# Kernel optimization log

Measured on AMD Instinct MI355X. Metric: run time of the kernel, lower is better.

Reference implementation:

```python
import jax, jax.numpy as jnp
import numpy as np

B, T, C = 4, 1024, 1024
N_HEAD = 16
MEMORY = 64  # sliding-window size: key j visible to query i iff 0 <= i-j <= MEMORY


def setup_inputs() -> dict:
    key = jax.random.key(0)
    k1, k2, k3 = jax.random.split(key, 3)
    x = jax.random.normal(k1, (B, T, C), dtype=jnp.float32)
    # torch Linear weight is [out, in]; we store transposed [in, out] for x @ W
    W_attn = jax.random.normal(k2, (C, 3 * C), dtype=jnp.float32) * (1.0 / np.sqrt(C))
    W_proj = jax.random.normal(k3, (C, C), dtype=jnp.float32) * (1.0 / np.sqrt(C))
    return {"x": x, "W_attn": W_attn, "W_proj": W_proj}


def reference(x, W_attn, W_proj):
    Bv, Tv, Cv = x.shape
    hd = Cv // N_HEAD
    qkv = x @ W_attn                               # [B,T,3C]
    q, k, v = jnp.split(qkv, 3, axis=-1)
    def heads(t):
        return t.reshape(Bv, Tv, N_HEAD, hd).transpose(0, 2, 1, 3)  # [B,H,T,hd]
    q, k, v = heads(q), heads(k), heads(v)
    scale = 1.0 / np.sqrt(hd)
    scores = jnp.einsum('bhqd,bhkd->bhqk', q, k) * scale            # [B,H,T,T]
    i = jnp.arange(Tv)
    diff = i[:, None] - i[None, :]                                  # i - j
    band_mask = (diff >= 0) & (diff <= MEMORY)                      # M1 * ~M2
    y = jax.nn.softmax(jnp.where(band_mask, scores, -jnp.inf), axis=-1) @ v
    # get_att=True path: full causal attention probabilities (no window)
    att = jax.nn.softmax(jnp.where(diff >= 0, scores, -jnp.inf), axis=-1)
    att_std = jnp.std(att, axis=0, ddof=1)                          # torch .std default ddof=1
    y = y.transpose(0, 2, 1, 3).reshape(Bv, Tv, Cv)
    y = y @ W_proj
    return (y, att, att_std)
```

## Files before the change

kernel.cpp:

```cpp
#include <hip/hip_runtime.h>
#include <hip/hip_bf16.h>
#include <stdint.h>

#define Bb 4
#define Tt 1024
#define Hh 16
#define HD 64
#define C3 3072
#define WIN 64

typedef __bf16 bf16x8 __attribute__((ext_vector_type(8)));
typedef float f32x4 __attribute__((ext_vector_type(4)));

#define MFMA16(a, b, c) __builtin_amdgcn_mfma_f32_16x16x32_bf16((a), (b), (c), 0, 0, 0)

static __device__ __forceinline__ unsigned short f2bf(float f) {
  union { float f; unsigned u; } v; v.f = f;
  unsigned r = (v.u + 0x7FFFu + ((v.u >> 16) & 1u)) >> 16;
  return (unsigned short)r;
}
static __device__ __forceinline__ float bf2f(unsigned short h) {
  union { unsigned u; float f; } v; v.u = ((unsigned)h) << 16;
  return v.f;
}

__global__ __launch_bounds__(256) void k_convert(const float* __restrict__ in,
                                                 unsigned short* __restrict__ out, int n4) {
  int i = blockIdx.x * 256 + threadIdx.x;
  if (i >= n4) return;
  float4 v = ((const float4*)in)[i];
  ushort4 o;
  o.x = f2bf(v.x); o.y = f2bf(v.y); o.z = f2bf(v.z); o.w = f2bf(v.w);
  ((ushort4*)out)[i] = o;
}

__global__ __launch_bounds__(256) void k_transconv(const float* __restrict__ Win,
                                                   unsigned short* __restrict__ Wt,
                                                   int K, int N) {
  __shared__ float tile[32][33];
  int n0 = blockIdx.x * 32, k0 = blockIdx.y * 32;
  int tx = threadIdx.x & 31, ty = threadIdx.x >> 5;
  for (int r = ty; r < 32; r += 8)
    tile[r][tx] = Win[(size_t)(k0 + r) * N + n0 + tx];
  __syncthreads();
  for (int r = ty; r < 32; r += 8)
    Wt[(size_t)(n0 + r) * K + k0 + tx] = f2bf(tile[tx][r]);
}

template <int BF16_OUT, int SCALEQ>
__global__ __launch_bounds__(256) void k_gemm_bt(const unsigned short* __restrict__ A,
                                                 const unsigned short* __restrict__ Bt,
                                                 void* __restrict__ Cv, int M, int N, int K) {
  __shared__ unsigned short lds[2 * 128 * 32];
  unsigned short* as_ = lds;
  unsigned short* bs_ = lds + 128 * 32;
  const int tid = threadIdx.x;
  const int m0 = blockIdx.x * 128, n0 = blockIdx.y * 128;
  const int w = tid >> 6, lane = tid & 63;
  const int wm = (w >> 1) * 64, wn = (w & 1) * 64;
  const int lrow = lane & 15, lk = lane >> 4;

  f32x4 z = {0.f, 0.f, 0.f, 0.f};
  f32x4 acc[4][4];
#pragma unroll
  for (int i = 0; i < 4; ++i)
#pragma unroll
    for (int j = 0; j < 4; ++j) acc[i][j] = z;

  const int nk = K >> 5;
  for (int kt = 0; kt < nk; ++kt) {
    const int k0 = kt << 5;
    __syncthreads();
#pragma unroll
    for (int p = 0; p < 2; ++p) {
      int seg = tid + p * 256;
      int row = seg >> 2, ks = (seg & 3) << 3;
      __builtin_amdgcn_global_load_lds(
          (__attribute__((address_space(1))) void*)(A + (size_t)(m0 + row) * K + k0 + ks),
          (__attribute__((address_space(3))) void*)(as_ + seg * 8), 16, 0, 0);
      __builtin_amdgcn_global_load_lds(
          (__attribute__((address_space(1))) void*)(Bt + (size_t)(n0 + row) * K + k0 + ks),
          (__attribute__((address_space(3))) void*)(bs_ + seg * 8), 16, 0, 0);
    }
    __syncthreads();
    bf16x8 af[4], bfr[4];
#pragma unroll
    for (int f = 0; f < 4; ++f) {
      af[f] = *(const bf16x8*)(as_ + (wm + f * 16 + lrow) * 32 + lk * 8);
      bfr[f] = *(const bf16x8*)(bs_ + (wn + f * 16 + lrow) * 32 + lk * 8);
    }
#pragma unroll
    for (int i = 0; i < 4; ++i)
#pragma unroll
      for (int j = 0; j < 4; ++j) acc[i][j] = MFMA16(af[i], bfr[j], acc[i][j]);
  }
  const int r0 = lk * 4;
#pragma unroll
  for (int i = 0; i < 4; ++i)
#pragma unroll
    for (int j = 0; j < 4; ++j)
#pragma unroll
      for (int r = 0; r < 4; ++r) {
        int gm = m0 + wm + i * 16 + r0 + r;
        int gn = n0 + wn + j * 16 + lrow;
        float v = acc[i][j][r];
        if (SCALEQ) {
          if (gn < 1024) v *= 0.125f;
        }
        if (BF16_OUT)
          ((unsigned short*)Cv)[(size_t)gm * N + gn] = f2bf(v);
        else
          ((float*)Cv)[(size_t)gm * N + gn] = v;
      }
}

__global__ __launch_bounds__(256) void k_att(const unsigned short* __restrict__ qkv,
                                             float* __restrict__ att, float* __restrict__ astd) {
  const int ti = blockIdx.x, h = blockIdx.y;
  const int i0 = ti * 32;
  const int tid = threadIdx.x;
  const int w = tid >> 6, lane = tid & 63;
  const int b = w;
  const int lrow = lane & 15, lk = lane >> 4;

  __shared__ float pbuf[4][32][36];

  const size_t qbase = ((size_t)(b * Tt + i0 + lrow)) * C3 + h * 64 + lk * 8;
  bf16x8 q00 = *(const bf16x8*)(qkv + qbase);
  bf16x8 q01 = *(const bf16x8*)(qkv + qbase + 32);
  bf16x8 q10 = *(const bf16x8*)(qkv + qbase + (size_t)16 * C3);
  bf16x8 q11 = *(const bf16x8*)(qkv + qbase + (size_t)16 * C3 + 32);

  float m[2][4], l[2][4];
#pragma unroll
  for (int i2 = 0; i2 < 2; ++i2)
#pragma unroll
    for (int r = 0; r < 4; ++r) { m[i2][r] = -1e30f; l[i2][r] = 0.f; }

  for (int jt = 0; jt <= ti; ++jt) {
    const int j0 = jt * 32;
    const size_t krowa = ((size_t)(b * Tt + j0 + lrow)) * C3 + 1024 + h * 64 + lk * 8;
    const size_t krowb = krowa + (size_t)16 * C3;
    bf16x8 k00 = *(const bf16x8*)(qkv + krowa);
    bf16x8 k01 = *(const bf16x8*)(qkv + krowa + 32);
    bf16x8 k10 = *(const bf16x8*)(qkv + krowb);
    bf16x8 k11 = *(const bf16x8*)(qkv + krowb + 32);
    const int ja = j0 + lrow, jb2 = j0 + 16 + lrow;
#pragma unroll
    for (int i2 = 0; i2 < 2; ++i2) {
      bf16x8 qa = i2 ? q10 : q00;
      bf16x8 qb = i2 ? q11 : q01;
      f32x4 sa = {0.f, 0.f, 0.f, 0.f}, sb = {0.f, 0.f, 0.f, 0.f};
      sa = MFMA16(qa, k00, sa);
      sa = MFMA16(qb, k01, sa);
      sb = MFMA16(qa, k10, sb);
      sb = MFMA16(qb, k11, sb);
#pragma unroll
      for (int r = 0; r < 4; ++r) {
        int ig = i0 + i2 * 16 + lk * 4 + r;
        int oka = (ja <= ig), okb = (jb2 <= ig);
        float va = oka ? sa[r] : -1e30f;
        float vb = okb ? sb[r] : -1e30f;
        float mn = fmaxf(m[i2][r], fmaxf(va, vb));
        float pa = oka ? __expf(sa[r] - mn) : 0.f;
        float pb = okb ? __expf(sb[r] - mn) : 0.f;
        l[i2][r] = l[i2][r] * __expf(m[i2][r] - mn) + pa + pb;
        m[i2][r] = mn;
      }
    }
  }
  float rl[2][4];
#pragma unroll
  for (int i2 = 0; i2 < 2; ++i2)
#pragma unroll
    for (int r = 0; r < 4; ++r) {
      float mm = m[i2][r], ll = l[i2][r];
#pragma unroll
      for (int d = 1; d <= 8; d <<= 1) {
        float mo = __shfl_xor(mm, d);
        float lo = __shfl_xor(ll, d);
        float mn = fmaxf(mm, mo);
        ll = ll * __expf(mm - mn) + lo * __expf(mo - mn);
        mm = mn;
      }
      m[i2][r] = mm;
      rl[i2][r] = 1.0f / ll;
    }

  const float4 z4 = make_float4(0.f, 0.f, 0.f, 0.f);
  for (int jt = 0; jt < 32; ++jt) {
    const int j0 = jt * 32;
    if (jt > ti) {
#pragma unroll
      for (int q = 0; q < 4; ++q) {
        int f = q * 64 + lane;
        int row = f >> 3, c4 = f & 7;
        *(float4*)&att[(((size_t)(b * Hh + h)) * Tt + i0 + row) * Tt + j0 + c4 * 4] = z4;
      }
      {
        int row = tid >> 3, c4 = tid & 7;
        *(float4*)&astd[((size_t)h * Tt + i0 + row) * Tt + j0 + c4 * 4] = z4;
      }
      continue;
    }
    const size_t krowa = ((size_t)(b * Tt + j0 + lrow)) * C3 + 1024 + h * 64 + lk * 8;
    const size_t krowb = krowa + (size_t)16 * C3;
    bf16x8 k00 = *(const bf16x8*)(qkv + krowa);
    bf16x8 k01 = *(const bf16x8*)(qkv + krowa + 32);
    bf16x8 k10 = *(const bf16x8*)(qkv + krowb);
    bf16x8 k11 = *(const bf16x8*)(qkv + krowb + 32);
#pragma unroll
    for (int i2 = 0; i2 < 2; ++i2) {
      bf16x8 qa = i2 ? q10 : q00;
      bf16x8 qb = i2 ? q11 : q01;
#pragma unroll
      for (int j2 = 0; j2 < 2; ++j2) {
        f32x4 s = {0.f, 0.f, 0.f, 0.f};
        s = MFMA16(qa, j2 ? k10 : k00, s);
        s = MFMA16(qb, j2 ? k11 : k01, s);
        const int jg = j0 + j2 * 16 + lrow;
#pragma unroll
        for (int r = 0; r < 4; ++r) {
          int ig = i0 + i2 * 16 + lk * 4 + r;
          float p = (jg <= ig) ? __expf(s[r] - m[i2][r]) * rl[i2][r] : 0.f;
          pbuf[b][i2 * 16 + lk * 4 + r][j2 * 16 + lrow] = p;
        }
      }
    }
#pragma unroll
    for (int q = 0; q < 4; ++q) {
      int f = q * 64 + lane;
      int row = f >> 3, c4 = f & 7;
      float4 v = *(float4*)&pbuf[b][row][c4 * 4];
      *(float4*)&att[(((size_t)(b * Hh + h)) * Tt + i0 + row) * Tt + j0 + c4 * 4] = v;
    }
    __syncthreads();
    {
      int row = tid >> 3, c4 = tid & 7;
      float4 p0 = *(float4*)&pbuf[0][row][c4 * 4];
      float4 p1 = *(float4*)&pbuf[1][row][c4 * 4];
      float4 p2 = *(float4*)&pbuf[2][row][c4 * 4];
      float4 p3 = *(float4*)&pbuf[3][row][c4 * 4];
      float4 o;
      float s1, mean, var;
      s1 = p0.x + p1.x + p2.x + p3.x; mean = s1 * 0.25f;
      var = (p0.x*p0.x + p1.x*p1.x + p2.x*p2.x + p3.x*p3.x - 4.f*mean*mean) * (1.f/3.f);
      o.x = sqrtf(fmaxf(var, 0.f));
      s1 = p0.y + p1.y + p2.y + p3.y; mean = s1 * 0.25f;
      var = (p0.y*p0.y + p1.y*p1.y + p2.y*p2.y + p3.y*p3.y - 4.f*mean*mean) * (1.f/3.f);
      o.y = sqrtf(fmaxf(var, 0.f));
      s1 = p0.z + p1.z + p2.z + p3.z; mean = s1 * 0.25f;
      var = (p0.z*p0.z + p1.z*p1.z + p2.z*p2.z + p3.z*p3.z - 4.f*mean*mean) * (1.f/3.f);
      o.z = sqrtf(fmaxf(var, 0.f));
      s1 = p0.w + p1.w + p2.w + p3.w; mean = s1 * 0.25f;
      var = (p0.w*p0.w + p1.w*p1.w + p2.w*p2.w + p3.w*p3.w - 4.f*mean*mean) * (1.f/3.f);
      o.w = sqrtf(fmaxf(var, 0.f));
      *(float4*)&astd[((size_t)h * Tt + i0 + row) * Tt + j0 + c4 * 4] = o;
    }
    __syncthreads();
  }
}

__global__ __launch_bounds__(256) void k_bandy(const unsigned short* __restrict__ qkv,
                                               unsigned short* __restrict__ yh) {
  __shared__ unsigned short qls[64 * 66];
  __shared__ unsigned short kls[128 * 66];
  __shared__ unsigned short vls[128 * 66];
  __shared__ float pls[4][80];

  int blk = blockIdx.x;
  int it = blk & 15, h = (blk >> 4) & 15, b = blk >> 8;
  int i0 = it * 64;
  int jb = i0 - 64;
  int tid = threadIdx.x;

  for (int r = tid; r < 320; r += 256) {
    unsigned short* dst;
    int grow, sel;
    if (r < 64) { dst = qls + r * 66; grow = i0 + r; sel = 0; }
    else if (r < 192) { dst = kls + (r - 64) * 66; grow = jb + (r - 64); sel = 1; }
    else { dst = vls + (r - 192) * 66; grow = jb + (r - 192); sel = 2; }
    if (grow < 0) {
      for (int t = 0; t < 32; ++t) ((unsigned*)dst)[t] = 0u;
    } else {
      const unsigned* src = (const unsigned*)(qkv + ((size_t)(b * Tt + grow)) * C3 + sel * 1024 + h * 64);
      for (int t = 0; t < 32; ++t) ((unsigned*)dst)[t] = src[t];
    }
  }
  __syncthreads();

  const int w = tid >> 6, lane = tid & 63;
  for (int rr = 0; rr < 16; ++rr) {
    const int i = i0 + (w << 4) + rr;
    const int io = i - i0;
    const int ja = i - 64 + lane;
    const unsigned* qrow = (const unsigned*)(qls + io * 66);
    const unsigned* krow = (const unsigned*)(kls + (size_t)(io + lane) * 66);
    const unsigned* kerow = (const unsigned*)(kls + (size_t)(io + 64) * 66);
    float sa = 0.f, se = 0.f;
#pragma unroll 8
    for (int t = 0; t < 32; ++t) {
      unsigned qq = qrow[t];
      float q0 = bf2f((unsigned short)qq), q1 = bf2f((unsigned short)(qq >> 16));
      unsigned kk = krow[t];
      sa = fmaf(q0, bf2f((unsigned short)kk), sa);
      sa = fmaf(q1, bf2f((unsigned short)(kk >> 16)), sa);
      unsigned ke = kerow[t];
      se = fmaf(q0, bf2f((unsigned short)ke), se);
      se = fmaf(q1, bf2f((unsigned short)(ke >> 16)), se);
    }
    if (ja < 0) sa = -1e30f;
    float m = sa;
    m = fmaxf(m, __shfl_xor(m, 1));
    m = fmaxf(m, __shfl_xor(m, 2));
    m = fmaxf(m, __shfl_xor(m, 4));
    m = fmaxf(m, __shfl_xor(m, 8));
    m = fmaxf(m, __shfl_xor(m, 16));
    m = fmaxf(m, __shfl_xor(m, 32));
    m = fmaxf(m, se);
    float pa = __expf(sa - m);
    float pe = __expf(se - m);
    float sum = pa;
    sum += __shfl_xor(sum, 1);
    sum += __shfl_xor(sum, 2);
    sum += __shfl_xor(sum, 4);
    sum += __shfl_xor(sum, 8);
    sum += __shfl_xor(sum, 16);
    sum += __shfl_xor(sum, 32);
    sum += pe;
    float rl = 1.0f / sum;
    pls[w][lane] = pa * rl;
    if (lane == 0) pls[w][64] = pe * rl;
    float y = 0.f;
#pragma unroll 4
    for (int t = 0; t <= 64; ++t)
      y = fmaf(pls[w][t], bf2f(vls[(size_t)(io + t) * 66 + lane]), y);
    yh[((size_t)(b * Tt + i)) * 1024 + h * 64 + lane] = f2bf(y);
  }
}

extern "C" void kernel_launch(void* const* d_in, const int* in_sizes, int n_in,
                              void* d_out, int out_size, void* d_ws, size_t ws_size,
                              hipStream_t stream) {
  const float* x = (const float*)d_in[0];
  const float* Wa = (const float*)d_in[1];
  const float* Wp = (const float*)d_in[2];

  float* out = (float*)d_out;
  float* y_out = out;
  float* att = out + (size_t)4194304;
  float* astd = out + (size_t)71303168;

  char* ws = (char*)d_ws;
  unsigned short* qkv = (unsigned short*)ws;
  unsigned short* yh = (unsigned short*)(ws + 25165824);
  unsigned short* WtP = (unsigned short*)(ws + 33554432);

  char* yreg = (char*)d_out;
  unsigned short* WtA = (unsigned short*)yreg;
  unsigned short* xbf = (unsigned short*)(yreg + 6291456);

  k_convert<<<4096, 256, 0, stream>>>(x, xbf, 1048576);
  k_transconv<<<dim3(96, 32), 256, 0, stream>>>(Wa, WtA, 1024, 3072);
  k_transconv<<<dim3(32, 32), 256, 0, stream>>>(Wp, WtP, 1024, 1024);
  k_gemm_bt<1, 1><<<dim3(32, 24), 256, 0, stream>>>(xbf, WtA, qkv, 4096, 3072, 1024);
  k_att<<<dim3(32, 16), 256, 0, stream>>>(qkv, att, astd);
  k_bandy<<<1024, 256, 0, stream>>>(qkv, yh);
  k_gemm_bt<0, 0><<<dim3(32, 8), 256, 0, stream>>>(yh, WtP, y_out, 4096, 1024, 1024);
}
```

Baseline: 309.6 us.

## Split att output tiles across warps and merge prep kernels into one launch

The prep step now runs as one kernel, replacing three launches (x conversion and two weight transposes). In the attention-probability kernel, each warp still computes softmax row statistics for one batch, then shares them through shared memory. The second pass is changed so each warp owns a subset of column tiles and handles all four batches, accumulating the std statistics in registers instead of synchronizing the whole block per tile. The row-tile order is also reversed so the longest blocks start first. This removes two block barriers per column tile and evens out the causal load imbalance, at the cost of more registers for the Q fragments of all batches.

```diff
diff --git a/kernel.cpp b/kernel.cpp
--- a/kernel.cpp
+++ b/kernel.cpp
@@ -24,22 +24,28 @@
   return v.f;
 }
 
-__global__ __launch_bounds__(256) void k_convert(const float* __restrict__ in,
-                                                 unsigned short* __restrict__ out, int n4) {
-  int i = blockIdx.x * 256 + threadIdx.x;
-  if (i >= n4) return;
-  float4 v = ((const float4*)in)[i];
-  ushort4 o;
-  o.x = f2bf(v.x); o.y = f2bf(v.y); o.z = f2bf(v.z); o.w = f2bf(v.w);
-  ((ushort4*)out)[i] = o;
-}
-
-__global__ __launch_bounds__(256) void k_transconv(const float* __restrict__ Win,
-                                                   unsigned short* __restrict__ Wt,
-                                                   int K, int N) {
+__global__ __launch_bounds__(256) void k_prep(const float* __restrict__ x,
+                                              const float* __restrict__ Wa,
+                                              const float* __restrict__ Wp,
+                                              unsigned short* __restrict__ xbf,
+                                              unsigned short* __restrict__ WtA,
+                                              unsigned short* __restrict__ WtP) {
   __shared__ float tile[32][33];
-  int n0 = blockIdx.x * 32, k0 = blockIdx.y * 32;
-  int tx = threadIdx.x & 31, ty = threadIdx.x >> 5;
+  const int blk = blockIdx.x;
+  const int tid = threadIdx.x;
+  if (blk < 4096) {
+    int i = blk * 256 + tid;
+    float4 v = ((const float4*)x)[i];
+    ushort4 o;
+    o.x = f2bf(v.x); o.y = f2bf(v.y); o.z = f2bf(v.z); o.w = f2bf(v.w);
+    ((ushort4*)xbf)[i] = o;
+    return;
+  }
+  const float* Win; unsigned short* Wt; int N, n0, k0;
+  if (blk < 7168) { int bb = blk - 4096; Win = Wa; Wt = WtA; N = 3072; n0 = (bb % 96) * 32; k0 = (bb / 96) * 32; }
+  else           { int bb = blk - 7168; Win = Wp; Wt = WtP; N = 1024; n0 = (bb % 32) * 32; k0 = (bb / 32) * 32; }
+  const int K = 1024;
+  int tx = tid & 31, ty = tid >> 5;
   for (int r = ty; r < 32; r += 8)
     tile[r][tx] = Win[(size_t)(k0 + r) * N + n0 + tx];
   __syncthreads();
@@ -116,148 +122,180 @@
 
 __global__ __launch_bounds__(256) void k_att(const unsigned short* __restrict__ qkv,
                                              float* __restrict__ att, float* __restrict__ astd) {
-  const int ti = blockIdx.x, h = blockIdx.y;
+  const int ti = 31 - blockIdx.x;
+  const int h = blockIdx.y;
   const int i0 = ti * 32;
   const int tid = threadIdx.x;
   const int w = tid >> 6, lane = tid & 63;
-  const int b = w;
   const int lrow = lane & 15, lk = lane >> 4;
 
-  __shared__ float pbuf[4][32][36];
-
-  const size_t qbase = ((size_t)(b * Tt + i0 + lrow)) * C3 + h * 64 + lk * 8;
-  bf16x8 q00 = *(const bf16x8*)(qkv + qbase);
-  bf16x8 q01 = *(const bf16x8*)(qkv + qbase + 32);
-  bf16x8 q10 = *(const bf16x8*)(qkv + qbase + (size_t)16 * C3);
-  bf16x8 q11 = *(const bf16x8*)(qkv + qbase + (size_t)16 * C3 + 32);
-
-  float m[2][4], l[2][4];
-#pragma unroll
-  for (int i2 = 0; i2 < 2; ++i2)
-#pragma unroll
-    for (int r = 0; r < 4; ++r) { m[i2][r] = -1e30f; l[i2][r] = 0.f; }
-
-  for (int jt = 0; jt <= ti; ++jt) {
-    const int j0 = jt * 32;
-    const size_t krowa = ((size_t)(b * Tt + j0 + lrow)) * C3 + 1024 + h * 64 + lk * 8;
-    const size_t krowb = krowa + (size_t)16 * C3;
-    bf16x8 k00 = *(const bf16x8*)(qkv + krowa);
-    bf16x8 k01 = *(const bf16x8*)(qkv + krowa + 32);
-    bf16x8 k10 = *(const bf16x8*)(qkv + krowb);
-    bf16x8 k11 = *(const bf16x8*)(qkv + krowb + 32);
-    const int ja = j0 + lrow, jb2 = j0 + 16 + lrow;
-#pragma unroll
-    for (int i2 = 0; i2 < 2; ++i2) {
-      bf16x8 qa = i2 ? q10 : q00;
-      bf16x8 qb = i2 ? q11 : q01;
-      f32x4 sa = {0.f, 0.f, 0.f, 0.f}, sb = {0.f, 0.f, 0.f, 0.f};
-      sa = MFMA16(qa, k00, sa);
-      sa = MFMA16(qb, k01, sa);
-      sb = MFMA16(qa, k10, sb);
-      sb = MFMA16(qb, k11, sb);
+  __shared__ float smr[4][32][2];
+  __shared__ float wbuf[4][32][36];
+
+  {
+    const int b1 = w;
+    const size_t qb_ = ((size_t)(b1 * Tt + i0 + lrow)) * C3 + h * 64 + lk * 8;
+    bf16x8 q00 = *(const bf16x8*)(qkv + qb_);
+    bf16x8 q01 = *(const bf16x8*)(qkv + qb_ + 32);
+    bf16x8 q10 = *(const bf16x8*)(qkv + qb_ + (size_t)16 * C3);
+    bf16x8 q11 = *(const bf16x8*)(qkv + qb_ + (size_t)16 * C3 + 32);
+
+    float m[2][4], l[2][4];
+#pragma unroll
+    for (int i2 = 0; i2 < 2; ++i2)
+#pragma unroll
+      for (int r = 0; r < 4; ++r) { m[i2][r] = -1e30f; l[i2][r] = 0.f; }
+
+    for (int jt = 0; jt <= ti; ++jt) {
+      const int j0 = jt * 32;
+      const size_t krowa = ((size_t)(b1 * Tt + j0 + lrow)) * C3 + 1024 + h * 64 + lk * 8;
+      const size_t krowb = krowa + (size_t)16 * C3;
+      bf16x8 k00 = *(const bf16x8*)(qkv + krowa);
+      bf16x8 k01 = *(const bf16x8*)(qkv + krowa + 32);
+      bf16x8 k10 = *(const bf16x8*)(qkv + krowb);
+      bf16x8 k11 = *(const bf16x8*)(qkv + krowb + 32);
+      const int ja = j0 + lrow, jb2 = j0 + 16 + lrow;
+#pragma unroll
+      for (int i2 = 0; i2 < 2; ++i2) {
+        bf16x8 qa = i2 ? q10 : q00;
+        bf16x8 qb = i2 ? q11 : q01;
+        f32x4 sa = {0.f, 0.f, 0.f, 0.f}, sb = {0.f, 0.f, 0.f, 0.f};
+        sa = MFMA16(qa, k00, sa);
+        sa = MFMA16(qb, k01, sa);
+        sb = MFMA16(qa, k10, sb);
+        sb = MFMA16(qb, k11, sb);
+#pragma unroll
+        for (int r = 0; r < 4; ++r) {
+          int ig = i0 + i2 * 16 + lk * 4 + r;
+          int oka = (ja <= ig), okb = (jb2 <= ig);
+          float va = oka ? sa[r] : -1e30f;
+          float vb = okb ? sb[r] : -1e30f;
+          float mn = fmaxf(m[i2][r], fmaxf(va, vb));
+          float pa = oka ? __expf(sa[r] - mn) : 0.f;
+          float pb = okb ? __expf(sb[r] - mn) : 0.f;
+          l[i2][r] = l[i2][r] * __expf(m[i2][r] - mn) + pa + pb;
+          m[i2][r] = mn;
+        }
+      }
+    }
+#pragma unroll
+    for (int i2 = 0; i2 < 2; ++i2)
 #pragma unroll
       for (int r = 0; r < 4; ++r) {
-        int ig = i0 + i2 * 16 + lk * 4 + r;
-        int oka = (ja <= ig), okb = (jb2 <= ig);
-        float va = oka ? sa[r] : -1e30f;
-        float vb = okb ? sb[r] : -1e30f;
-        float mn = fmaxf(m[i2][r], fmaxf(va, vb));
-        float pa = oka ? __expf(sa[r] - mn) : 0.f;
-        float pb = okb ? __expf(sb[r] - mn) : 0.f;
-        l[i2][r] = l[i2][r] * __expf(m[i2][r] - mn) + pa + pb;
-        m[i2][r] = mn;
-      }
-    }
-  }
-  float rl[2][4];
-#pragma unroll
-  for (int i2 = 0; i2 < 2; ++i2)
-#pragma unroll
-    for (int r = 0; r < 4; ++r) {
-      float mm = m[i2][r], ll = l[i2][r];
-#pragma unroll
-      for (int d = 1; d <= 8; d <<= 1) {
-        float mo = __shfl_xor(mm, d);
-        float lo = __shfl_xor(ll, d);
-        float mn = fmaxf(mm, mo);
-        ll = ll * __expf(mm - mn) + lo * __expf(mo - mn);
-        mm = mn;
-      }
-      m[i2][r] = mm;
-      rl[i2][r] = 1.0f / ll;
-    }
+        float mm = m[i2][r], ll = l[i2][r];
+#pragma unroll
+        for (int d = 1; d <= 8; d <<= 1) {
+          float mo = __shfl_xor(mm, d);
+          float lo = __shfl_xor(ll, d);
+          float mn = fmaxf(mm, mo);
+          ll = ll * __expf(mm - mn) + lo * __expf(mo - mn);
+          mm = mn;
+        }
+        if (lrow == 0) {
+          int row = i2 * 16 + lk * 4 + r;
+          smr[b1][row][0] = mm;
+          smr[b1][row][1] = 1.0f / ll;
+        }
+      }
+  }
+  __syncthreads();
+
+  bf16x8 qf[4][2][2];
+#pragma unroll
+  for (int b = 0; b < 4; ++b) {
+    const size_t qb_ = ((size_t)(b * Tt + i0 + lrow)) * C3 + h * 64 + lk * 8;
+    qf[b][0][0] = *(const bf16x8*)(qkv + qb_);
+    qf[b][0][1] = *(const bf16x8*)(qkv + qb_ + 32);
+    qf[b][1][0] = *(const bf16x8*)(qkv + qb_ + (size_t)16 * C3);
+    qf[b][1][1] = *(const bf16x8*)(qkv + qb_ + (size_t)16 * C3 + 32);
+  }
 
   const float4 z4 = make_float4(0.f, 0.f, 0.f, 0.f);
-  for (int jt = 0; jt < 32; ++jt) {
+  for (int jt = w; jt < 32; jt += 4) {
     const int j0 = jt * 32;
     if (jt > ti) {
+#pragma unroll
+      for (int b = 0; b < 4; ++b)
+#pragma unroll
+        for (int q = 0; q < 4; ++q) {
+          int f = q * 64 + lane;
+          int row = f >> 3, c4 = f & 7;
+          *(float4*)&att[(((size_t)(b * Hh + h)) * Tt + i0 + row) * Tt + j0 + c4 * 4] = z4;
+        }
 #pragma unroll
       for (int q = 0; q < 4; ++q) {
         int f = q * 64 + lane;
         int row = f >> 3, c4 = f & 7;
-        *(float4*)&att[(((size_t)(b * Hh + h)) * Tt + i0 + row) * Tt + j0 + c4 * 4] = z4;
-      }
-      {
-        int row = tid >> 3, c4 = tid & 7;
         *(float4*)&astd[((size_t)h * Tt + i0 + row) * Tt + j0 + c4 * 4] = z4;
       }
       continue;
     }
-    const size_t krowa = ((size_t)(b * Tt + j0 + lrow)) * C3 + 1024 + h * 64 + lk * 8;
-    const size_t krowb = krowa + (size_t)16 * C3;
-    bf16x8 k00 = *(const bf16x8*)(qkv + krowa);
-    bf16x8 k01 = *(const bf16x8*)(qkv + krowa + 32);
-    bf16x8 k10 = *(const bf16x8*)(qkv + krowb);
-    bf16x8 k11 = *(const bf16x8*)(qkv + krowb + 32);
-#pragma unroll
-    for (int i2 = 0; i2 < 2; ++i2) {
-      bf16x8 qa = i2 ? q10 : q00;
-      bf16x8 qb = i2 ? q11 : q01;
-#pragma unroll
-      for (int j2 = 0; j2 < 2; ++j2) {
-        f32x4 s = {0.f, 0.f, 0.f, 0.f};
-        s = MFMA16(qa, j2 ? k10 : k00, s);
-        s = MFMA16(qb, j2 ? k11 : k01, s);
-        const int jg = j0 + j2 * 16 + lrow;
+    float s1[2][2][4], s2[2][2][4];
+#pragma unroll
+    for (int i2 = 0; i2 < 2; ++i2)
+#pragma unroll
+      for (int j2 = 0; j2 < 2; ++j2)
+#pragma unroll
+        for (int r = 0; r < 4; ++r) { s1[i2][j2][r] = 0.f; s2[i2][j2][r] = 0.f; }
+
+#pragma unroll
+    for (int b = 0; b < 4; ++b) {
+      const size_t krowa = ((size_t)(b * Tt + j0 + lrow)) * C3 + 1024 + h * 64 + lk * 8;
+      const size_t krowb = krowa + (size_t)16 * C3;
+      bf16x8 k00 = *(const bf16x8*)(qkv + krowa);
+      bf16x8 k01 = *(const bf16x8*)(qkv + krowa + 32);
+      bf16x8 k10 = *(const bf16x8*)(qkv + krowb);
+      bf16x8 k11 = *(const bf16x8*)(qkv + krowb + 32);
+#pragma unroll
+      for (int i2 = 0; i2 < 2; ++i2) {
+        float mm[4], rr[4];
 #pragma unroll
         for (int r = 0; r < 4; ++r) {
-          int ig = i0 + i2 * 16 + lk * 4 + r;
-          float p = (jg <= ig) ? __expf(s[r] - m[i2][r]) * rl[i2][r] : 0.f;
-          pbuf[b][i2 * 16 + lk * 4 + r][j2 * 16 + lrow] = p;
-        }
-      }
-    }
+          int row = i2 * 16 + lk * 4 + r;
+          mm[r] = smr[b][row][0];
+          rr[r] = smr[b][row][1];
+        }
+#pragma unroll
+        for (int j2 = 0; j2 < 2; ++j2) {
+          f32x4 s = {0.f, 0.f, 0.f, 0.f};
+          s = MFMA16(qf[b][i2][0], j2 ? k10 : k00, s);
+          s = MFMA16(qf[b][i2][1], j2 ? k11 : k01, s);
+          const int jg = j0 + j2 * 16 + lrow;
+#pragma unroll
+          for (int r = 0; r < 4; ++r) {
+            int ig = i0 + i2 * 16 + lk * 4 + r;
+            float p = (jg <= ig) ? __expf(s[r] - mm[r]) * rr[r] : 0.f;
+            wbuf[w][i2 * 16 + lk * 4 + r][j2 * 16 + lrow] = p;
+            s1[i2][j2][r] += p;
+            s2[i2][j2][r] += p * p;
+          }
+        }
+      }
+#pragma unroll
+      for (int q = 0; q < 4; ++q) {
+        int f = q * 64 + lane;
+        int row = f >> 3, c4 = f & 7;
+        float4 v = *(float4*)&wbuf[w][row][c4 * 4];
+        *(float4*)&att[(((size_t)(b * Hh + h)) * Tt + i0 + row) * Tt + j0 + c4 * 4] = v;
+      }
+    }
+#pragma unroll
+    for (int i2 = 0; i2 < 2; ++i2)
+#pragma unroll
+      for (int j2 = 0; j2 < 2; ++j2)
+#pragma unroll
+        for (int r = 0; r < 4; ++r) {
+          float mean = s1[i2][j2][r] * 0.25f;
+          float var = (s2[i2][j2][r] - 4.f * mean * mean) * (1.f / 3.f);
+          wbuf[w][i2 * 16 + lk * 4 + r][j2 * 16 + lrow] = sqrtf(fmaxf(var, 0.f));
+        }
 #pragma unroll
     for (int q = 0; q < 4; ++q) {
       int f = q * 64 + lane;
       int row = f >> 3, c4 = f & 7;
-      float4 v = *(float4*)&pbuf[b][row][c4 * 4];
-      *(float4*)&att[(((size_t)(b * Hh + h)) * Tt + i0 + row) * Tt + j0 + c4 * 4] = v;
-    }
-    __syncthreads();
-    {
-      int row = tid >> 3, c4 = tid & 7;
-      float4 p0 = *(float4*)&pbuf[0][row][c4 * 4];
-      float4 p1 = *(float4*)&pbuf[1][row][c4 * 4];
-      float4 p2 = *(float4*)&pbuf[2][row][c4 * 4];
-      float4 p3 = *(float4*)&pbuf[3][row][c4 * 4];
-      float4 o;
-      float s1, mean, var;
-      s1 = p0.x + p1.x + p2.x + p3.x; mean = s1 * 0.25f;
-      var = (p0.x*p0.x + p1.x*p1.x + p2.x*p2.x + p3.x*p3.x - 4.f*mean*mean) * (1.f/3.f);
-      o.x = sqrtf(fmaxf(var, 0.f));
-      s1 = p0.y + p1.y + p2.y + p3.y; mean = s1 * 0.25f;
-      var = (p0.y*p0.y + p1.y*p1.y + p2.y*p2.y + p3.y*p3.y - 4.f*mean*mean) * (1.f/3.f);
-      o.y = sqrtf(fmaxf(var, 0.f));
-      s1 = p0.z + p1.z + p2.z + p3.z; mean = s1 * 0.25f;
-      var = (p0.z*p0.z + p1.z*p1.z + p2.z*p2.z + p3.z*p3.z - 4.f*mean*mean) * (1.f/3.f);
-      o.z = sqrtf(fmaxf(var, 0.f));
-      s1 = p0.w + p1.w + p2.w + p3.w; mean = s1 * 0.25f;
-      var = (p0.w*p0.w + p1.w*p1.w + p2.w*p2.w + p3.w*p3.w - 4.f*mean*mean) * (1.f/3.f);
-      o.w = sqrtf(fmaxf(var, 0.f));
-      *(float4*)&astd[((size_t)h * Tt + i0 + row) * Tt + j0 + c4 * 4] = o;
-    }
-    __syncthreads();
+      float4 v = *(float4*)&wbuf[w][row][c4 * 4];
+      *(float4*)&astd[((size_t)h * Tt + i0 + row) * Tt + j0 + c4 * 4] = v;
+    }
   }
 }
 
@@ -360,9 +398,7 @@
   unsigned short* WtA = (unsigned short*)yreg;
   unsigned short* xbf = (unsigned short*)(yreg + 6291456);
 
-  k_convert<<<4096, 256, 0, stream>>>(x, xbf, 1048576);
-  k_transconv<<<dim3(96, 32), 256, 0, stream>>>(Wa, WtA, 1024, 3072);
-  k_transconv<<<dim3(32, 32), 256, 0, stream>>>(Wp, WtP, 1024, 1024);
+  k_prep<<<8192, 256, 0, stream>>>(x, Wa, Wp, xbf, WtA, WtP);
   k_gemm_bt<1, 1><<<dim3(32, 24), 256, 0, stream>>>(xbf, WtA, qkv, 4096, 3072, 1024);
   k_att<<<dim3(32, 16), 256, 0, stream>>>(qkv, att, astd);
   k_bandy<<<1024, 256, 0, stream>>>(qkv, yh);
```

After: 295.6 us. 1.05x faster.
